# Performance work log

Hardware: AMD Instinct MI355X
Metric: run time of the kernel (lower is better)

Reference implementation:

```python
import jax, jax.numpy as jnp
import numpy as np

N_NODES = 100000
N_EDGES = 1600000
IN_DIM = 128
HID_DIM = 128
OUT_DIM = 64
BN_EPS = 1e-5


def setup_inputs() -> dict:
    key = jax.random.key(0)
    ks = jax.random.split(key, 8)
    x = jax.random.normal(ks[0], (N_NODES, IN_DIM), dtype=jnp.float32)
    edge_index = jax.random.randint(ks[1], (2, N_EDGES), 0, N_NODES, dtype=jnp.int64)
    s1 = 1.0 / np.sqrt(IN_DIM)
    s2 = 1.0 / np.sqrt(HID_DIM)
    return {
        "x": x,
        "edge_index": edge_index,
        "W1l": jax.random.normal(ks[2], (HID_DIM, IN_DIM), dtype=jnp.float32) * s1,
        "b1l": jnp.zeros((HID_DIM,), dtype=jnp.float32),
        "W1r": jax.random.normal(ks[3], (HID_DIM, IN_DIM), dtype=jnp.float32) * s1,
        "bn_gamma": jnp.ones((HID_DIM,), dtype=jnp.float32),
        "bn_beta": jnp.zeros((HID_DIM,), dtype=jnp.float32),
        "bn_mean": jnp.zeros((HID_DIM,), dtype=jnp.float32),
        "bn_var": jnp.ones((HID_DIM,), dtype=jnp.float32),
        "W2l": jax.random.normal(ks[4], (OUT_DIM, HID_DIM), dtype=jnp.float32) * s2,
        "b2l": jnp.zeros((OUT_DIM,), dtype=jnp.float32),
        "W2r": jax.random.normal(ks[5], (OUT_DIM, HID_DIM), dtype=jnp.float32) * s2,
    }


def _sage_conv(x, src, dst, Wl, bl, Wr, num_nodes):
    # message = x[src], mean-aggregated at dst; out = lin_l(agg) + lin_r(x)
    msgs = x[src]  # [E, D] gather (memory bound)
    agg = jax.ops.segment_sum(msgs, dst, num_segments=num_nodes)
    deg = jax.ops.segment_sum(jnp.ones((src.shape[0],), dtype=x.dtype), dst,
                              num_segments=num_nodes)
    agg = agg / jnp.maximum(deg, 1.0)[:, None]
    return agg @ Wl.T + bl + x @ Wr.T


def reference(x, edge_index, W1l, b1l, W1r, bn_gamma, bn_beta, bn_mean, bn_var,
              W2l, b2l, W2r):
    src, dst = edge_index[0], edge_index[1]
    n = x.shape[0]
    h = _sage_conv(x, src, dst, W1l, b1l, W1r, n)
    # BatchNorm1d (inference: running stats), then ReLU; dropout is identity in eval
    h = (h - bn_mean) * (bn_gamma * jax.lax.rsqrt(bn_var + BN_EPS)) + bn_beta
    h = jax.nn.relu(h)
    return _sage_conv(h, src, dst, W2l, b2l, W2r, n)
```

## Files before the change

### kernel.cpp

```cpp
#include <hip/hip_runtime.h>
#include <hip/hip_fp16.h>

#define N_NODES 100000
#define N_EDGES 1600000
#define TILE 2048
#define NBUK 64
#define BSH 11
#define NBUK_USED ((N_NODES + (1 << BSH) - 1) >> BSH)
#define CAP 36864
#define SMASK 0x1FFFF

typedef _Float16 f16x8 __attribute__((ext_vector_type(8)));
typedef float    f32x4 __attribute__((ext_vector_type(4)));

__global__ __launch_bounds__(64) void k_binit(int* __restrict__ bcur)
{
    int t = threadIdx.x;
    if (t < NBUK) bcur[t] = t * CAP;
}

__global__ __launch_bounds__(256) void k_binA(
    const int* __restrict__ ei, int* __restrict__ bcur,
    int2* __restrict__ ebuf)
{
    __shared__ int2 scratch[TILE];
    __shared__ int hist[NBUK];
    __shared__ int tstart[NBUK];
    __shared__ int gbase[NBUK];
    int t = threadIdx.x;
    int e0 = blockIdx.x * TILE;
    int tile_n = min(TILE, N_EDGES - e0);
    if (t < NBUK) hist[t] = 0;
    __syncthreads();
    int srcs[8], dsts[8], rank[8], bks[8];
    #pragma unroll
    for (int i = 0; i < 8; ++i) {
        int e = e0 + i * 256 + t;
        bks[i] = -1;
        if (e < N_EDGES) {
            srcs[i] = ei[e];
            dsts[i] = ei[N_EDGES + e];
            bks[i]  = (dsts[i] >> BSH) & (NBUK - 1);
            rank[i] = atomicAdd(&hist[bks[i]], 1);
        }
    }
    __syncthreads();
    if (t == 0) {
        int s = 0;
        #pragma unroll
        for (int b = 0; b < NBUK; ++b) { tstart[b] = s; s += hist[b]; }
    }
    __syncthreads();
    if (t < NBUK && hist[t] > 0)
        gbase[t] = atomicAdd(&bcur[t], hist[t]);
    __syncthreads();
    #pragma unroll
    for (int i = 0; i < 8; ++i)
        if (bks[i] >= 0) {
            int sl = tstart[bks[i]] + rank[i];
            scratch[min(sl, TILE - 1)] = make_int2(srcs[i], dsts[i]);
        }
    __syncthreads();
    for (int p = t; p < tile_n; p += 256) {
        int2 sd = scratch[p];
        int b = (sd.y >> BSH) & (NBUK - 1);
        int o = gbase[b] + (p - tstart[b]);
        ebuf[min(max(o, 0), NBUK * CAP - 1)] = sd;
    }
}

__global__ __launch_bounds__(64) void k_scanb(
    const int* __restrict__ bcur, int* __restrict__ bbase)
{
    __shared__ int s[64];
    int t = threadIdx.x;
    int c = (t < NBUK_USED) ? (bcur[t] - t * CAP) : 0;
    c = min(max(c, 0), CAP);
    s[t] = c;
    __syncthreads();
    #pragma unroll
    for (int off = 1; off < 64; off <<= 1) {
        int v = (t >= off) ? s[t - off] : 0;
        __syncthreads();
        s[t] += v;
        __syncthreads();
    }
    if (t < NBUK_USED) bbase[t] = s[t] - c;
    if (t == NBUK_USED - 1) bbase[NBUK_USED] = s[t];
}

__global__ __launch_bounds__(1024) void k_fillC2(
    const int2* __restrict__ ebuf, const int* __restrict__ bbase,
    int* __restrict__ row_ptr, int* __restrict__ csr_src)
{
    __shared__ int hist[1 << BSH];
    __shared__ int psum[1024];
    __shared__ int cur[1 << BSH];
    int t = threadIdx.x;
    int b = blockIdx.x;
    int base = b << BSH;
    hist[t] = 0;
    hist[t + 1024] = 0;
    __syncthreads();
    int bb  = bbase[b];
    int cnt = min(bbase[b + 1] - bb, CAP);
    const int2* eb = ebuf + (size_t)b * CAP;
    for (int p = t; p < cnt; p += 1024)
        atomicAdd(&hist[(eb[p].y - base) & ((1 << BSH) - 1)], 1);
    __syncthreads();
    int h0 = hist[2 * t], h1 = hist[2 * t + 1];
    psum[t] = h0 + h1;
    __syncthreads();
    #pragma unroll
    for (int off = 1; off < 1024; off <<= 1) {
        int v = (t >= off) ? psum[t - off] : 0;
        __syncthreads();
        psum[t] += v;
        __syncthreads();
    }
    int e0 = bb + psum[t] - (h0 + h1);
    int e1 = e0 + h0;
    int n0g = base + 2 * t, n1g = n0g + 1;
    if (n0g <= N_NODES) row_ptr[n0g] = e0;
    if (n1g <= N_NODES) row_ptr[n1g] = e1;
    cur[2 * t]     = e0;
    cur[2 * t + 1] = e1;
    __syncthreads();
    for (int p = t; p < cnt; p += 1024) {
        int2 sd = eb[p];
        int pos = atomicAdd(&cur[(sd.y - base) & ((1 << BSH) - 1)], 1);
        csr_src[min(max(pos, 0), N_EDGES - 1)] = sd.x;
    }
}

__global__ __launch_bounds__(256) void k_tohalf(
    const float* __restrict__ x, __half* __restrict__ x_h)
{
    int i = blockIdx.x * 256 + threadIdx.x;
    if (i < N_NODES * 32) {
        float4 v = ((const float4*)x)[i];
        __half2 a = __floats2half2_rn(v.x, v.y);
        __half2 b = __floats2half2_rn(v.z, v.w);
        uint2 u = make_uint2(*(unsigned*)&a, *(unsigned*)&b);
        ((uint2*)x_h)[i] = u;
    }
}

__global__ __launch_bounds__(256) void k_wfrag(
    const float* __restrict__ W1l, const float* __restrict__ W1r,
    const float* __restrict__ W2l, const float* __restrict__ W2r,
    __half* __restrict__ W1lf, __half* __restrict__ W1rf,
    __half* __restrict__ W2f)
{
    int t = blockIdx.x * 256 + threadIdx.x;
    if (t >= 49152) return;
    int tt = t & 16383;
    int j    = tt & 7;
    int lane = (tt >> 3) & 63;
    int ks   = (tt >> 9) & 3;
    int ct   = tt >> 11;
    int m = lane & 15, q = lane >> 4;
    int row = ct * 16 + m;
    int col = ks * 32 + q * 8 + j;
    if (t < 16384) {
        W1lf[tt] = __float2half(W1l[row * 128 + col]);
    } else if (t < 32768) {
        W1rf[tt] = __float2half(W1r[row * 128 + col]);
    } else {
        float v = (ct < 4) ? W2l[row * 128 + col]
                           : W2r[(row - 64) * 128 + col];
        W2f[tt] = __float2half(v);
    }
}

__device__ __forceinline__ void acc_row_h(
    const __half* __restrict__ x_h, int s, int lane, float4& acc)
{
    uint2 u = ((const uint2*)(x_h + (size_t)(s & SMASK) * 128))[lane];
    __half2 a = *(__half2*)&u.x;
    __half2 b = *(__half2*)&u.y;
    float2 fa = __half22float2(a);
    float2 fb = __half22float2(b);
    acc.x += fa.x; acc.y += fa.y; acc.z += fb.x; acc.w += fb.y;
}

__global__ __launch_bounds__(256) void k_agg1(
    const int* __restrict__ row_ptr, const int* __restrict__ csr_src,
    const __half* __restrict__ x_h, __half* __restrict__ agg_h)
{
    int tid  = threadIdx.x;
    int n    = blockIdx.x * 8 + (tid >> 5);
    int lane = tid & 31;
    int e1 = min(row_ptr[n + 1], N_EDGES);
    int e0 = min(max(row_ptr[n], 0), e1);
    float4 acc = make_float4(0.f, 0.f, 0.f, 0.f);
    int e = e0;
    for (; e + 4 <= e1; e += 4) {
        int s0 = csr_src[e], s1 = csr_src[e + 1];
        int s2 = csr_src[e + 2], s3 = csr_src[e + 3];
        acc_row_h(x_h, s0, lane, acc);
        acc_row_h(x_h, s1, lane, acc);
        acc_row_h(x_h, s2, lane, acc);
        acc_row_h(x_h, s3, lane, acc);
    }
    for (; e < e1; ++e) acc_row_h(x_h, csr_src[e], lane, acc);
    __half2 h0 = __floats2half2_rn(acc.x, acc.y);
    __half2 h1 = __floats2half2_rn(acc.z, acc.w);
    uint2 u = make_uint2(*(unsigned*)&h0, *(unsigned*)&h1);
    ((uint2*)agg_h)[n * 32 + lane] = u;
}

__global__ __launch_bounds__(256) void k_gemm1(
    const __half* __restrict__ agg_h, const int* __restrict__ row_ptr,
    const __half* __restrict__ x_h,
    const __half* __restrict__ W1lf, const float* __restrict__ b1l,
    const __half* __restrict__ W1rf,
    const float* __restrict__ gamma, const float* __restrict__ beta,
    const float* __restrict__ mean, const float* __restrict__ var,
    __half* __restrict__ h_h)
{
    __shared__ char sm[32768];
    __half (*Aagg)[64][8] = (__half(*)[64][8])sm;
    __half (*Ax)[64][8]   = (__half(*)[64][8])(sm + 16384);
    __half (*Hs)[136]     = (__half(*)[136])sm;
    int tid = threadIdx.x;
    int n0  = blockIdx.x * 64;
    {
        int n  = tid & 63;
        int kg = tid >> 6;
        int ng = n0 + n;
        const uint4* pa = (const uint4*)(agg_h + (size_t)ng * 128 + kg * 32);
        const uint4* px = (const uint4*)(x_h   + (size_t)ng * 128 + kg * 32);
        #pragma unroll
        for (int i = 0; i < 4; ++i) {
            uint4 va = make_uint4(0, 0, 0, 0), vx = va;
            if (ng < N_NODES) { va = pa[i]; vx = px[i]; }
            *(uint4*)&Aagg[kg * 4 + i][n][0] = va;
            *(uint4*)&Ax[kg * 4 + i][n][0]   = vx;
        }
    }
    __syncthreads();
    int lane = tid & 63;
    int w = tid >> 6;
    int m = lane & 15;
    int q = lane >> 4;
    int row = w * 16 + m;
    const __half* bl0 = W1lf + (lane << 3);
    const __half* br0 = W1rf + (lane << 3);
    f32x4 accL[8], accR[8];
    #pragma unroll
    for (int c = 0; c < 8; ++c) {
        accL[c] = (f32x4){0.f, 0.f, 0.f, 0.f};
        accR[c] = (f32x4){0.f, 0.f, 0.f, 0.f};
    }
    #pragma unroll
    for (int ks = 0; ks < 4; ++ks) {
        f16x8 aL = *(const f16x8*)&Aagg[ks * 4 + q][row][0];
        f16x8 aR = *(const f16x8*)&Ax[ks * 4 + q][row][0];
        #pragma unroll
        for (int ct = 0; ct < 8; ++ct) {
            f16x8 bL = *(const f16x8*)(bl0 + ((ct * 4 + ks) << 9));
            f16x8 bR = *(const f16x8*)(br0 + ((ct * 4 + ks) << 9));
            accL[ct] = __builtin_amdgcn_mfma_f32_16x16x32_f16(aL, bL, accL[ct], 0, 0, 0);
            accR[ct] = __builtin_amdgcn_mfma_f32_16x16x32_f16(aR, bR, accR[ct], 0, 0, 0);
        }
    }
    float invd[4];
    #pragma unroll
    for (int r = 0; r < 4; ++r) {
        int n = n0 + w * 16 + q * 4 + r;
        int d = (n < N_NODES) ? (row_ptr[n + 1] - row_ptr[n]) : 1;
        invd[r] = 1.0f / fmaxf((float)d, 1.0f);
    }
    __syncthreads();
    #pragma unroll
    for (int ct = 0; ct < 8; ++ct) {
        int col = ct * 16 + m;
        float s = gamma[col] * rsqrtf(var[col] + 1e-5f);
        float t = beta[col] + (b1l[col] - mean[col]) * s;
        #pragma unroll
        for (int r = 0; r < 4; ++r) {
            float v = accL[ct][r] * invd[r] + accR[ct][r];
            v = fmaxf(v * s + t, 0.f);
            Hs[w * 16 + q * 4 + r][col] = __float2half(v);
        }
    }
    __syncthreads();
    {
        int rr = tid & 63;
        int pg = tid >> 6;
        int ng = n0 + rr;
        if (ng < N_NODES) {
            uint4* dst = (uint4*)(h_h + (size_t)ng * 128);
            #pragma unroll
            for (int i = 0; i < 4; ++i)
                dst[pg * 4 + i] = *(const uint4*)&Hs[rr][(pg * 4 + i) * 8];
        }
    }
}

__global__ __launch_bounds__(256) void k_gemm2(
    const __half* __restrict__ h_h,
    const __half* __restrict__ W2f, const float* __restrict__ b2l,
    __half* __restrict__ p2, float* __restrict__ out)
{
    __shared__ char sm[33792];
    __half (*Ah)[64][8] = (__half(*)[64][8])sm;
    float  (*Cs)[132]   = (float(*)[132])sm;
    int tid = threadIdx.x;
    int n0  = blockIdx.x * 64;
    {
        int n  = tid & 63;
        int kg = tid >> 6;
        int ng = n0 + n;
        const uint4* ph = (const uint4*)(h_h + (size_t)ng * 128 + kg * 32);
        #pragma unroll
        for (int i = 0; i < 4; ++i) {
            uint4 vh = make_uint4(0, 0, 0, 0);
            if (ng < N_NODES) vh = ph[i];
            *(uint4*)&Ah[kg * 4 + i][n][0] = vh;
        }
    }
    __syncthreads();
    int lane = tid & 63;
    int w = tid >> 6;
    int m = lane & 15;
    int q = lane >> 4;
    int row = w * 16 + m;
    const __half* b0 = W2f + (lane << 3);
    f32x4 acc[8];
    #pragma unroll
    for (int c = 0; c < 8; ++c) acc[c] = (f32x4){0.f, 0.f, 0.f, 0.f};
    #pragma unroll
    for (int ks = 0; ks < 4; ++ks) {
        f16x8 a = *(const f16x8*)&Ah[ks * 4 + q][row][0];
        #pragma unroll
        for (int ct = 0; ct < 8; ++ct) {
            f16x8 b = *(const f16x8*)(b0 + ((ct * 4 + ks) << 9));
            acc[ct] = __builtin_amdgcn_mfma_f32_16x16x32_f16(a, b, acc[ct], 0, 0, 0);
        }
    }
    __syncthreads();
    #pragma unroll
    for (int ct = 0; ct < 8; ++ct) {
        int col = ct * 16 + m;
        #pragma unroll
        for (int r = 0; r < 4; ++r)
            Cs[w * 16 + q * 4 + r][col] = acc[ct][r];
    }
    __syncthreads();
    {
        int rr = tid & 63;
        int pg = tid >> 6;
        int ng = n0 + rr;
        if (ng < N_NODES) {
            union { __half hh[16]; uint4 u[2]; } tmp;
            #pragma unroll
            for (int c = 0; c < 16; ++c)
                tmp.hh[c] = __float2half(Cs[rr][pg * 16 + c]);
            uint4* dp = (uint4*)(p2 + (size_t)ng * 64 + pg * 16);
            dp[0] = tmp.u[0];
            dp[1] = tmp.u[1];
            #pragma unroll
            for (int i = 0; i < 4; ++i) {
                float4 v  = *(const float4*)&Cs[rr][64 + pg * 16 + i * 4];
                float4 bb = *(const float4*)(b2l + pg * 16 + i * 4);
                v.x += bb.x; v.y += bb.y; v.z += bb.z; v.w += bb.w;
                *(float4*)(out + (size_t)ng * 64 + pg * 16 + i * 4) = v;
            }
        }
    }
}

__device__ __forceinline__ void acc_row_p2(
    const __half* __restrict__ p2, int s, int lane, float4& acc)
{
    uint2 u = ((const uint2*)(p2 + (size_t)(s & SMASK) * 64))[lane];
    __half2 a = *(__half2*)&u.x;
    __half2 b = *(__half2*)&u.y;
    float2 fa = __half22float2(a);
    float2 fb = __half22float2(b);
    acc.x += fa.x; acc.y += fa.y; acc.z += fb.x; acc.w += fb.y;
}

__global__ __launch_bounds__(256) void k_agg2(
    const int* __restrict__ row_ptr, const int* __restrict__ csr_src,
    const __half* __restrict__ p2, float* __restrict__ out)
{
    int tid  = threadIdx.x;
    int n    = blockIdx.x * 16 + (tid >> 4);
    int lane = tid & 15;
    int e1 = min(row_ptr[n + 1], N_EDGES);
    int e0 = min(max(row_ptr[n], 0), e1);
    float4 acc = make_float4(0.f, 0.f, 0.f, 0.f);
    int e = e0;
    for (; e + 4 <= e1; e += 4) {
        int s0 = csr_src[e], s1 = csr_src[e + 1];
        int s2 = csr_src[e + 2], s3 = csr_src[e + 3];
        acc_row_p2(p2, s0, lane, acc);
        acc_row_p2(p2, s1, lane, acc);
        acc_row_p2(p2, s2, lane, acc);
        acc_row_p2(p2, s3, lane, acc);
    }
    for (; e < e1; ++e) acc_row_p2(p2, csr_src[e], lane, acc);
    float inv = 1.0f / fmaxf((float)(e1 - e0), 1.0f);
    float4* o = (float4*)out + n * 16 + lane;
    float4 cur = *o;
    cur.x += acc.x * inv; cur.y += acc.y * inv;
    cur.z += acc.z * inv; cur.w += acc.w * inv;
    *o = cur;
}

extern "C" void kernel_launch(void* const* d_in, const int* in_sizes, int n_in,
                              void* d_out, int out_size, void* d_ws, size_t ws_size,
                              hipStream_t stream)
{
    const float* x     = (const float*)d_in[0];
    const int*   ei    = (const int*)d_in[1];
    const float* W1l   = (const float*)d_in[2];
    const float* b1l   = (const float*)d_in[3];
    const float* W1r   = (const float*)d_in[4];
    const float* gamma = (const float*)d_in[5];
    const float* beta  = (const float*)d_in[6];
    const float* mean  = (const float*)d_in[7];
    const float* var   = (const float*)d_in[8];
    const float* W2l   = (const float*)d_in[9];
    const float* b2l   = (const float*)d_in[10];
    const float* W2r   = (const float*)d_in[11];
    float* out = (float*)d_out;

    char* ws = (char*)d_ws;
    __half* agg_h   = (__half*)(ws);
    __half* h_h     = (__half*)(ws + 25600000);
    __half* x_h     = (__half*)(ws + 51200000);
    int*    csr_src = (int*)(ws + 76800000);
    int*    row_ptr = (int*)(ws + 83200000);
    __half* W1lf    = (__half*)(ws + 83600016);
    __half* W1rf    = (__half*)(ws + 83632784);
    __half* W2f     = (__half*)(ws + 83665552);
    int2*   ebuf    = (int2*)(ws + 83698320);
    int*    bcur    = (int*)(ws + 102572688);
    int*    bbase   = (int*)(ws + 102572944);
    __half* p2      = agg_h;

    k_binit<<<1, 64, 0, stream>>>(bcur);
    k_tohalf<<<(N_NODES * 32 + 255) / 256, 256, 0, stream>>>(x, x_h);
    k_wfrag<<<192, 256, 0, stream>>>(W1l, W1r, W2l, W2r, W1lf, W1rf, W2f);
    k_binA<<<(N_EDGES + TILE - 1) / TILE, 256, 0, stream>>>(ei, bcur, ebuf);
    k_scanb<<<1, 64, 0, stream>>>(bcur, bbase);
    k_fillC2<<<NBUK_USED, 1024, 0, stream>>>(ebuf, bbase, row_ptr, csr_src);
    k_agg1<<<N_NODES / 8, 256, 0, stream>>>(row_ptr, csr_src, x_h, agg_h);
    k_gemm1<<<(N_NODES + 63) / 64, 256, 0, stream>>>(agg_h, row_ptr, x_h,
                                                     W1lf, b1l, W1rf,
                                                     gamma, beta, mean, var, h_h);
    k_gemm2<<<(N_NODES + 63) / 64, 256, 0, stream>>>(h_h, W2f, b2l, p2, out);
    k_agg2<<<N_NODES / 16, 256, 0, stream>>>(row_ptr, csr_src, p2, out);
}
```

Baseline: 335.4 us.

## Assign one wavefront per node in aggregation kernels with readlane-broadcast indices

Both gather-aggregation kernels now give each destination node a full 64-lane wavefront instead of 32 or 16 lanes. Edge indices are loaded cooperatively, one per lane, and broadcast with readlane. Lane groups then process different edges in parallel and are combined with xor shuffles at the end. The aim is more memory-level parallelism and fewer serialized dependent index loads per node. In exchange there is extra select and shuffle overhead, lanes sit partly idle on odd tails, and the grids are 2x and 4x larger.

```diff
diff --git a/kernel.cpp b/kernel.cpp
--- a/kernel.cpp
+++ b/kernel.cpp
@@ -173,10 +173,10 @@
     }
 }
 
-__device__ __forceinline__ void acc_row_h(
-    const __half* __restrict__ x_h, int s, int lane, float4& acc)
-{
-    uint2 u = ((const uint2*)(x_h + (size_t)(s & SMASK) * 128))[lane];
+__device__ __forceinline__ void acc_row8(
+    const __half* __restrict__ x_h, int s, int col, float4& acc)
+{
+    uint2 u = ((const uint2*)(x_h + (size_t)(s & SMASK) * 128))[col];
     __half2 a = *(__half2*)&u.x;
     __half2 b = *(__half2*)&u.y;
     float2 fa = __half22float2(a);
@@ -189,25 +189,47 @@
     const __half* __restrict__ x_h, __half* __restrict__ agg_h)
 {
     int tid  = threadIdx.x;
-    int n    = blockIdx.x * 8 + (tid >> 5);
-    int lane = tid & 31;
+    int lane = tid & 63;
+    int half = lane >> 5;
+    int col  = lane & 31;
+    int n    = blockIdx.x * 4 + (tid >> 6);
     int e1 = min(row_ptr[n + 1], N_EDGES);
     int e0 = min(max(row_ptr[n], 0), e1);
     float4 acc = make_float4(0.f, 0.f, 0.f, 0.f);
-    int e = e0;
-    for (; e + 4 <= e1; e += 4) {
-        int s0 = csr_src[e], s1 = csr_src[e + 1];
-        int s2 = csr_src[e + 2], s3 = csr_src[e + 3];
-        acc_row_h(x_h, s0, lane, acc);
-        acc_row_h(x_h, s1, lane, acc);
-        acc_row_h(x_h, s2, lane, acc);
-        acc_row_h(x_h, s3, lane, acc);
-    }
-    for (; e < e1; ++e) acc_row_h(x_h, csr_src[e], lane, acc);
-    __half2 h0 = __floats2half2_rn(acc.x, acc.y);
-    __half2 h1 = __floats2half2_rn(acc.z, acc.w);
-    uint2 u = make_uint2(*(unsigned*)&h0, *(unsigned*)&h1);
-    ((uint2*)agg_h)[n * 32 + lane] = u;
+    for (int eb = e0; eb < e1; eb += 64) {
+        int cnt = min(e1 - eb, 64);
+        int sv = csr_src[min(eb + lane, N_EDGES - 1)];
+        int j = 0;
+        for (; j + 8 <= cnt; j += 8) {
+            #pragma unroll
+            for (int u = 0; u < 4; ++u) {
+                int sa = __builtin_amdgcn_readlane(sv, j + 2 * u);
+                int sb = __builtin_amdgcn_readlane(sv, j + 2 * u + 1);
+                int s  = half ? sb : sa;
+                acc_row8(x_h, s, col, acc);
+            }
+        }
+        for (; j + 2 <= cnt; j += 2) {
+            int sa = __builtin_amdgcn_readlane(sv, j);
+            int sb = __builtin_amdgcn_readlane(sv, j + 1);
+            int s  = half ? sb : sa;
+            acc_row8(x_h, s, col, acc);
+        }
+        if (j < cnt) {
+            int sa = __builtin_amdgcn_readlane(sv, j);
+            if (half == 0) acc_row8(x_h, sa, col, acc);
+        }
+    }
+    acc.x += __shfl_xor(acc.x, 32);
+    acc.y += __shfl_xor(acc.y, 32);
+    acc.z += __shfl_xor(acc.z, 32);
+    acc.w += __shfl_xor(acc.w, 32);
+    if (half == 0) {
+        __half2 h0 = __floats2half2_rn(acc.x, acc.y);
+        __half2 h1 = __floats2half2_rn(acc.z, acc.w);
+        uint2 u = make_uint2(*(unsigned*)&h0, *(unsigned*)&h1);
+        ((uint2*)agg_h)[n * 32 + col] = u;
+    }
 }
 
 __global__ __launch_bounds__(256) void k_gemm1(
@@ -372,10 +394,10 @@
     }
 }
 
-__device__ __forceinline__ void acc_row_p2(
-    const __half* __restrict__ p2, int s, int lane, float4& acc)
-{
-    uint2 u = ((const uint2*)(p2 + (size_t)(s & SMASK) * 64))[lane];
+__device__ __forceinline__ void acc_row8p(
+    const __half* __restrict__ p2, int s, int col, float4& acc)
+{
+    uint2 u = ((const uint2*)(p2 + (size_t)(s & SMASK) * 64))[col];
     __half2 a = *(__half2*)&u.x;
     __half2 b = *(__half2*)&u.y;
     float2 fa = __half22float2(a);
@@ -388,27 +410,70 @@
     const __half* __restrict__ p2, float* __restrict__ out)
 {
     int tid  = threadIdx.x;
-    int n    = blockIdx.x * 16 + (tid >> 4);
-    int lane = tid & 15;
+    int lane = tid & 63;
+    int grp  = lane >> 4;
+    int col  = lane & 15;
+    int n    = blockIdx.x * 4 + (tid >> 6);
     int e1 = min(row_ptr[n + 1], N_EDGES);
     int e0 = min(max(row_ptr[n], 0), e1);
     float4 acc = make_float4(0.f, 0.f, 0.f, 0.f);
-    int e = e0;
-    for (; e + 4 <= e1; e += 4) {
-        int s0 = csr_src[e], s1 = csr_src[e + 1];
-        int s2 = csr_src[e + 2], s3 = csr_src[e + 3];
-        acc_row_p2(p2, s0, lane, acc);
-        acc_row_p2(p2, s1, lane, acc);
-        acc_row_p2(p2, s2, lane, acc);
-        acc_row_p2(p2, s3, lane, acc);
-    }
-    for (; e < e1; ++e) acc_row_p2(p2, csr_src[e], lane, acc);
-    float inv = 1.0f / fmaxf((float)(e1 - e0), 1.0f);
-    float4* o = (float4*)out + n * 16 + lane;
-    float4 cur = *o;
-    cur.x += acc.x * inv; cur.y += acc.y * inv;
-    cur.z += acc.z * inv; cur.w += acc.w * inv;
-    *o = cur;
+    for (int eb = e0; eb < e1; eb += 64) {
+        int cnt = min(e1 - eb, 64);
+        int sv = csr_src[min(eb + lane, N_EDGES - 1)];
+        int j = 0;
+        for (; j + 8 <= cnt; j += 8) {
+            #pragma unroll
+            for (int u = 0; u < 2; ++u) {
+                int s0 = __builtin_amdgcn_readlane(sv, j + 4 * u);
+                int s1 = __builtin_amdgcn_readlane(sv, j + 4 * u + 1);
+                int s2 = __builtin_amdgcn_readlane(sv, j + 4 * u + 2);
+                int s3 = __builtin_amdgcn_readlane(sv, j + 4 * u + 3);
+                int sl = (grp & 1) ? s1 : s0;
+                int sh = (grp & 1) ? s3 : s2;
+                int s  = (grp & 2) ? sh : sl;
+                acc_row8p(p2, s, col, acc);
+            }
+        }
+        for (; j + 4 <= cnt; j += 4) {
+            int s0 = __builtin_amdgcn_readlane(sv, j);
+            int s1 = __builtin_amdgcn_readlane(sv, j + 1);
+            int s2 = __builtin_amdgcn_readlane(sv, j + 2);
+            int s3 = __builtin_amdgcn_readlane(sv, j + 3);
+            int sl = (grp & 1) ? s1 : s0;
+            int sh = (grp & 1) ? s3 : s2;
+            int s  = (grp & 2) ? sh : sl;
+            acc_row8p(p2, s, col, acc);
+        }
+        if (j + 2 <= cnt) {
+            int s0 = __builtin_amdgcn_readlane(sv, j);
+            int s1 = __builtin_amdgcn_readlane(sv, j + 1);
+            if (grp < 2) {
+                int s = (grp & 1) ? s1 : s0;
+                acc_row8p(p2, s, col, acc);
+            }
+            j += 2;
+        }
+        if (j < cnt) {
+            int s0 = __builtin_amdgcn_readlane(sv, j);
+            if (grp == 0) acc_row8p(p2, s0, col, acc);
+        }
+    }
+    acc.x += __shfl_xor(acc.x, 16);
+    acc.y += __shfl_xor(acc.y, 16);
+    acc.z += __shfl_xor(acc.z, 16);
+    acc.w += __shfl_xor(acc.w, 16);
+    acc.x += __shfl_xor(acc.x, 32);
+    acc.y += __shfl_xor(acc.y, 32);
+    acc.z += __shfl_xor(acc.z, 32);
+    acc.w += __shfl_xor(acc.w, 32);
+    if (lane < 16) {
+        float inv = 1.0f / fmaxf((float)(e1 - e0), 1.0f);
+        float4* o = (float4*)out + n * 16 + col;
+        float4 cur = *o;
+        cur.x += acc.x * inv; cur.y += acc.y * inv;
+        cur.z += acc.z * inv; cur.w += acc.w * inv;
+        *o = cur;
+    }
 }
 
 extern "C" void kernel_launch(void* const* d_in, const int* in_sizes, int n_in,
@@ -449,10 +514,10 @@
     k_binA<<<(N_EDGES + TILE - 1) / TILE, 256, 0, stream>>>(ei, bcur, ebuf);
     k_scanb<<<1, 64, 0, stream>>>(bcur, bbase);
     k_fillC2<<<NBUK_USED, 1024, 0, stream>>>(ebuf, bbase, row_ptr, csr_src);
-    k_agg1<<<N_NODES / 8, 256, 0, stream>>>(row_ptr, csr_src, x_h, agg_h);
+    k_agg1<<<N_NODES / 4, 256, 0, stream>>>(row_ptr, csr_src, x_h, agg_h);
     k_gemm1<<<(N_NODES + 63) / 64, 256, 0, stream>>>(agg_h, row_ptr, x_h,
                                                      W1lf, b1l, W1rf,
                                                      gamma, beta, mean, var, h_h);
     k_gemm2<<<(N_NODES + 63) / 64, 256, 0, stream>>>(h_h, W2f, b2l, p2, out);
-    k_agg2<<<N_NODES / 16, 256, 0, stream>>>(row_ptr, csr_src, p2, out);
-}
+    k_agg2<<<N_NODES / 4, 256, 0, stream>>>(row_ptr, csr_src, p2, out);
+}
```

Result: slower. 343.2 us (+2.3%).

## Fuse layer-1 aggregation with both GEMMs and merge setup kernels

Applied to the files above, without the earlier changes.

Merges the x-to-half conversion, weight fragment packing and bucket init into one pre-kernel, and folds the bucket-offset scan into the CSR fill kernel as a wave-shuffle scan. Layer-1 neighbour aggregation, the layer-1 GEMM with BN/ReLU, and the layer-2 GEMM now run in one kernel, so agg_h and h_h never go through global memory and the per-node degree is computed in-kernel. The new aggregation uses 64 nodes per block, with each wave handling 16 nodes serially and the two half-waves taking alternating edges. This removes kernel launches and intermediate round-trips, but it may lower the memory-level parallelism of the gather phase and adds shared-memory pressure.

```diff
diff --git a/kernel.cpp b/kernel.cpp
--- a/kernel.cpp
+++ b/kernel.cpp
@@ -13,10 +13,41 @@
 typedef _Float16 f16x8 __attribute__((ext_vector_type(8)));
 typedef float    f32x4 __attribute__((ext_vector_type(4)));
 
-__global__ __launch_bounds__(64) void k_binit(int* __restrict__ bcur)
-{
-    int t = threadIdx.x;
-    if (t < NBUK) bcur[t] = t * CAP;
+__global__ __launch_bounds__(256) void k_pre(
+    const float* __restrict__ x, __half* __restrict__ x_h,
+    const float* __restrict__ W1l, const float* __restrict__ W1r,
+    const float* __restrict__ W2l, const float* __restrict__ W2r,
+    __half* __restrict__ W1lf, __half* __restrict__ W1rf,
+    __half* __restrict__ W2f, int* __restrict__ bcur)
+{
+    int i = blockIdx.x * 256 + threadIdx.x;
+    if (i < N_NODES * 32) {
+        float4 v = ((const float4*)x)[i];
+        __half2 a = __floats2half2_rn(v.x, v.y);
+        __half2 b = __floats2half2_rn(v.z, v.w);
+        uint2 u = make_uint2(*(unsigned*)&a, *(unsigned*)&b);
+        ((uint2*)x_h)[i] = u;
+    }
+    if (i < 49152) {
+        int tt = i & 16383;
+        int j    = tt & 7;
+        int lane = (tt >> 3) & 63;
+        int ks   = (tt >> 9) & 3;
+        int ct   = tt >> 11;
+        int m = lane & 15, q = lane >> 4;
+        int row = ct * 16 + m;
+        int col = ks * 32 + q * 8 + j;
+        if (i < 16384) {
+            W1lf[tt] = __float2half(W1l[row * 128 + col]);
+        } else if (i < 32768) {
+            W1rf[tt] = __float2half(W1r[row * 128 + col]);
+        } else {
+            float v = (ct < 4) ? W2l[row * 128 + col]
+                               : W2r[(row - 64) * 128 + col];
+            W2f[tt] = __float2half(v);
+        }
+    }
+    if (i < NBUK) bcur[i] = i * CAP;
 }
 
 __global__ __launch_bounds__(256) void k_binA(
@@ -69,41 +100,34 @@
     }
 }
 
-__global__ __launch_bounds__(64) void k_scanb(
-    const int* __restrict__ bcur, int* __restrict__ bbase)
-{
-    __shared__ int s[64];
-    int t = threadIdx.x;
-    int c = (t < NBUK_USED) ? (bcur[t] - t * CAP) : 0;
-    c = min(max(c, 0), CAP);
-    s[t] = c;
-    __syncthreads();
-    #pragma unroll
-    for (int off = 1; off < 64; off <<= 1) {
-        int v = (t >= off) ? s[t - off] : 0;
-        __syncthreads();
-        s[t] += v;
-        __syncthreads();
-    }
-    if (t < NBUK_USED) bbase[t] = s[t] - c;
-    if (t == NBUK_USED - 1) bbase[NBUK_USED] = s[t];
-}
-
 __global__ __launch_bounds__(1024) void k_fillC2(
-    const int2* __restrict__ ebuf, const int* __restrict__ bbase,
+    const int2* __restrict__ ebuf, const int* __restrict__ bcur,
     int* __restrict__ row_ptr, int* __restrict__ csr_src)
 {
     __shared__ int hist[1 << BSH];
     __shared__ int psum[1024];
     __shared__ int cur[1 << BSH];
+    __shared__ int bb_l[NBUK_USED + 1];
     int t = threadIdx.x;
     int b = blockIdx.x;
     int base = b << BSH;
     hist[t] = 0;
     hist[t + 1024] = 0;
-    __syncthreads();
-    int bb  = bbase[b];
-    int cnt = min(bbase[b + 1] - bb, CAP);
+    if (t < 64) {
+        int c = (t < NBUK_USED) ? (bcur[t] - t * CAP) : 0;
+        c = min(max(c, 0), CAP);
+        int s = c;
+        #pragma unroll
+        for (int off = 1; off < 64; off <<= 1) {
+            int v = __shfl_up(s, off);
+            if (t >= off) s += v;
+        }
+        if (t < NBUK_USED) bb_l[t] = s - c;
+        if (t == NBUK_USED - 1) bb_l[NBUK_USED] = s;
+    }
+    __syncthreads();
+    int bb  = bb_l[b];
+    int cnt = min(bb_l[b + 1] - bb, CAP);
     const int2* eb = ebuf + (size_t)b * CAP;
     for (int p = t; p < cnt; p += 1024)
         atomicAdd(&hist[(eb[p].y - base) & ((1 << BSH) - 1)], 1);
@@ -133,50 +157,10 @@
     }
 }
 
-__global__ __launch_bounds__(256) void k_tohalf(
-    const float* __restrict__ x, __half* __restrict__ x_h)
-{
-    int i = blockIdx.x * 256 + threadIdx.x;
-    if (i < N_NODES * 32) {
-        float4 v = ((const float4*)x)[i];
-        __half2 a = __floats2half2_rn(v.x, v.y);
-        __half2 b = __floats2half2_rn(v.z, v.w);
-        uint2 u = make_uint2(*(unsigned*)&a, *(unsigned*)&b);
-        ((uint2*)x_h)[i] = u;
-    }
-}
-
-__global__ __launch_bounds__(256) void k_wfrag(
-    const float* __restrict__ W1l, const float* __restrict__ W1r,
-    const float* __restrict__ W2l, const float* __restrict__ W2r,
-    __half* __restrict__ W1lf, __half* __restrict__ W1rf,
-    __half* __restrict__ W2f)
-{
-    int t = blockIdx.x * 256 + threadIdx.x;
-    if (t >= 49152) return;
-    int tt = t & 16383;
-    int j    = tt & 7;
-    int lane = (tt >> 3) & 63;
-    int ks   = (tt >> 9) & 3;
-    int ct   = tt >> 11;
-    int m = lane & 15, q = lane >> 4;
-    int row = ct * 16 + m;
-    int col = ks * 32 + q * 8 + j;
-    if (t < 16384) {
-        W1lf[tt] = __float2half(W1l[row * 128 + col]);
-    } else if (t < 32768) {
-        W1rf[tt] = __float2half(W1r[row * 128 + col]);
-    } else {
-        float v = (ct < 4) ? W2l[row * 128 + col]
-                           : W2r[(row - 64) * 128 + col];
-        W2f[tt] = __float2half(v);
-    }
-}
-
-__device__ __forceinline__ void acc_row_h(
-    const __half* __restrict__ x_h, int s, int lane, float4& acc)
-{
-    uint2 u = ((const uint2*)(x_h + (size_t)(s & SMASK) * 128))[lane];
+__device__ __forceinline__ void acc_row8(
+    const __half* __restrict__ x_h, int s, int col, float4& acc)
+{
+    uint2 u = ((const uint2*)(x_h + (size_t)(s & SMASK) * 128))[col];
     __half2 a = *(__half2*)&u.x;
     __half2 b = *(__half2*)&u.y;
     float2 fa = __half22float2(a);
@@ -184,64 +168,91 @@
     acc.x += fa.x; acc.y += fa.y; acc.z += fb.x; acc.w += fb.y;
 }
 
-__global__ __launch_bounds__(256) void k_agg1(
+__global__ __launch_bounds__(256) void k_l12(
     const int* __restrict__ row_ptr, const int* __restrict__ csr_src,
-    const __half* __restrict__ x_h, __half* __restrict__ agg_h)
-{
-    int tid  = threadIdx.x;
-    int n    = blockIdx.x * 8 + (tid >> 5);
-    int lane = tid & 31;
-    int e1 = min(row_ptr[n + 1], N_EDGES);
-    int e0 = min(max(row_ptr[n], 0), e1);
-    float4 acc = make_float4(0.f, 0.f, 0.f, 0.f);
-    int e = e0;
-    for (; e + 4 <= e1; e += 4) {
-        int s0 = csr_src[e], s1 = csr_src[e + 1];
-        int s2 = csr_src[e + 2], s3 = csr_src[e + 3];
-        acc_row_h(x_h, s0, lane, acc);
-        acc_row_h(x_h, s1, lane, acc);
-        acc_row_h(x_h, s2, lane, acc);
-        acc_row_h(x_h, s3, lane, acc);
-    }
-    for (; e < e1; ++e) acc_row_h(x_h, csr_src[e], lane, acc);
-    __half2 h0 = __floats2half2_rn(acc.x, acc.y);
-    __half2 h1 = __floats2half2_rn(acc.z, acc.w);
-    uint2 u = make_uint2(*(unsigned*)&h0, *(unsigned*)&h1);
-    ((uint2*)agg_h)[n * 32 + lane] = u;
-}
-
-__global__ __launch_bounds__(256) void k_gemm1(
-    const __half* __restrict__ agg_h, const int* __restrict__ row_ptr,
     const __half* __restrict__ x_h,
     const __half* __restrict__ W1lf, const float* __restrict__ b1l,
     const __half* __restrict__ W1rf,
     const float* __restrict__ gamma, const float* __restrict__ beta,
     const float* __restrict__ mean, const float* __restrict__ var,
-    __half* __restrict__ h_h)
-{
-    __shared__ char sm[32768];
+    const __half* __restrict__ W2f, const float* __restrict__ b2l,
+    __half* __restrict__ p2, float* __restrict__ out)
+{
+    __shared__ char sm[34816];
     __half (*Aagg)[64][8] = (__half(*)[64][8])sm;
     __half (*Ax)[64][8]   = (__half(*)[64][8])(sm + 16384);
-    __half (*Hs)[136]     = (__half(*)[136])sm;
-    int tid = threadIdx.x;
-    int n0  = blockIdx.x * 64;
+    __half (*Ah)[64][8]   = (__half(*)[64][8])sm;
+    float  (*Cs)[132]     = (float(*)[132])sm;
+    __shared__ float invdeg[64];
+    int tid  = threadIdx.x;
+    int lane = tid & 63;
+    int w    = tid >> 6;
+    int n0   = blockIdx.x * 64;
+
     {
         int n  = tid & 63;
         int kg = tid >> 6;
         int ng = n0 + n;
-        const uint4* pa = (const uint4*)(agg_h + (size_t)ng * 128 + kg * 32);
-        const uint4* px = (const uint4*)(x_h   + (size_t)ng * 128 + kg * 32);
+        const uint4* px = (const uint4*)(x_h + (size_t)ng * 128 + kg * 32);
         #pragma unroll
         for (int i = 0; i < 4; ++i) {
-            uint4 va = make_uint4(0, 0, 0, 0), vx = va;
-            if (ng < N_NODES) { va = pa[i]; vx = px[i]; }
-            *(uint4*)&Aagg[kg * 4 + i][n][0] = va;
-            *(uint4*)&Ax[kg * 4 + i][n][0]   = vx;
-        }
-    }
-    __syncthreads();
-    int lane = tid & 63;
-    int w = tid >> 6;
+            uint4 vx = make_uint4(0, 0, 0, 0);
+            if (ng < N_NODES) vx = px[i];
+            *(uint4*)&Ax[kg * 4 + i][n][0] = vx;
+        }
+    }
+
+    {
+        int half = lane >> 5;
+        int col  = lane & 31;
+        for (int i = 0; i < 16; ++i) {
+            int nn = n0 + w * 16 + i;
+            int e0 = 0, e1 = 0;
+            if (nn < N_NODES) {
+                e1 = min(row_ptr[nn + 1], N_EDGES);
+                e0 = min(max(row_ptr[nn], 0), e1);
+            }
+            float4 acc = make_float4(0.f, 0.f, 0.f, 0.f);
+            for (int eb = e0; eb < e1; eb += 64) {
+                int cnt = min(e1 - eb, 64);
+                int sv = csr_src[min(eb + lane, N_EDGES - 1)];
+                int j = 0;
+                for (; j + 8 <= cnt; j += 8) {
+                    #pragma unroll
+                    for (int u = 0; u < 4; ++u) {
+                        int sa = __builtin_amdgcn_readlane(sv, j + 2 * u);
+                        int sb = __builtin_amdgcn_readlane(sv, j + 2 * u + 1);
+                        int s  = half ? sb : sa;
+                        acc_row8(x_h, s, col, acc);
+                    }
+                }
+                for (; j + 2 <= cnt; j += 2) {
+                    int sa = __builtin_amdgcn_readlane(sv, j);
+                    int sb = __builtin_amdgcn_readlane(sv, j + 1);
+                    int s  = half ? sb : sa;
+                    acc_row8(x_h, s, col, acc);
+                }
+                if (j < cnt) {
+                    int sa = __builtin_amdgcn_readlane(sv, j);
+                    if (half == 0) acc_row8(x_h, sa, col, acc);
+                }
+            }
+            acc.x += __shfl_xor(acc.x, 32);
+            acc.y += __shfl_xor(acc.y, 32);
+            acc.z += __shfl_xor(acc.z, 32);
+            acc.w += __shfl_xor(acc.w, 32);
+            if (lane == 0)
+                invdeg[w * 16 + i] = 1.0f / fmaxf((float)(e1 - e0), 1.0f);
+            if (half == 0) {
+                __half2 h0 = __floats2half2_rn(acc.x, acc.y);
+                __half2 h1 = __floats2half2_rn(acc.z, acc.w);
+                uint2 u = make_uint2(*(unsigned*)&h0, *(unsigned*)&h1);
+                *(uint2*)&Aagg[col >> 1][w * 16 + i][(col & 1) * 4] = u;
+            }
+        }
+    }
+    __syncthreads();
+
     int m = lane & 15;
     int q = lane >> 4;
     int row = w * 16 + m;
@@ -267,12 +278,10 @@
     }
     float invd[4];
     #pragma unroll
-    for (int r = 0; r < 4; ++r) {
-        int n = n0 + w * 16 + q * 4 + r;
-        int d = (n < N_NODES) ? (row_ptr[n + 1] - row_ptr[n]) : 1;
-        invd[r] = 1.0f / fmaxf((float)d, 1.0f);
-    }
-    __syncthreads();
+    for (int r = 0; r < 4; ++r)
+        invd[r] = invdeg[w * 16 + q * 4 + r];
+    __syncthreads();
+
     #pragma unroll
     for (int ct = 0; ct < 8; ++ct) {
         int col = ct * 16 + m;
@@ -282,62 +291,22 @@
         for (int r = 0; r < 4; ++r) {
             float v = accL[ct][r] * invd[r] + accR[ct][r];
             v = fmaxf(v * s + t, 0.f);
-            Hs[w * 16 + q * 4 + r][col] = __float2half(v);
-        }
-    }
-    __syncthreads();
-    {
-        int rr = tid & 63;
-        int pg = tid >> 6;
-        int ng = n0 + rr;
-        if (ng < N_NODES) {
-            uint4* dst = (uint4*)(h_h + (size_t)ng * 128);
-            #pragma unroll
-            for (int i = 0; i < 4; ++i)
-                dst[pg * 4 + i] = *(const uint4*)&Hs[rr][(pg * 4 + i) * 8];
-        }
-    }
-}
-
-__global__ __launch_bounds__(256) void k_gemm2(
-    const __half* __restrict__ h_h,
-    const __half* __restrict__ W2f, const float* __restrict__ b2l,
-    __half* __restrict__ p2, float* __restrict__ out)
-{
-    __shared__ char sm[33792];
-    __half (*Ah)[64][8] = (__half(*)[64][8])sm;
-    float  (*Cs)[132]   = (float(*)[132])sm;
-    int tid = threadIdx.x;
-    int n0  = blockIdx.x * 64;
-    {
-        int n  = tid & 63;
-        int kg = tid >> 6;
-        int ng = n0 + n;
-        const uint4* ph = (const uint4*)(h_h + (size_t)ng * 128 + kg * 32);
-        #pragma unroll
-        for (int i = 0; i < 4; ++i) {
-            uint4 vh = make_uint4(0, 0, 0, 0);
-            if (ng < N_NODES) vh = ph[i];
-            *(uint4*)&Ah[kg * 4 + i][n][0] = vh;
-        }
-    }
-    __syncthreads();
-    int lane = tid & 63;
-    int w = tid >> 6;
-    int m = lane & 15;
-    int q = lane >> 4;
-    int row = w * 16 + m;
+            Ah[col >> 3][w * 16 + q * 4 + r][col & 7] = __float2half(v);
+        }
+    }
+    __syncthreads();
+
     const __half* b0 = W2f + (lane << 3);
-    f32x4 acc[8];
-    #pragma unroll
-    for (int c = 0; c < 8; ++c) acc[c] = (f32x4){0.f, 0.f, 0.f, 0.f};
+    f32x4 acc2[8];
+    #pragma unroll
+    for (int c = 0; c < 8; ++c) acc2[c] = (f32x4){0.f, 0.f, 0.f, 0.f};
     #pragma unroll
     for (int ks = 0; ks < 4; ++ks) {
         f16x8 a = *(const f16x8*)&Ah[ks * 4 + q][row][0];
         #pragma unroll
         for (int ct = 0; ct < 8; ++ct) {
             f16x8 b = *(const f16x8*)(b0 + ((ct * 4 + ks) << 9));
-            acc[ct] = __builtin_amdgcn_mfma_f32_16x16x32_f16(a, b, acc[ct], 0, 0, 0);
+            acc2[ct] = __builtin_amdgcn_mfma_f32_16x16x32_f16(a, b, acc2[ct], 0, 0, 0);
         }
     }
     __syncthreads();
@@ -346,7 +315,7 @@
         int col = ct * 16 + m;
         #pragma unroll
         for (int r = 0; r < 4; ++r)
-            Cs[w * 16 + q * 4 + r][col] = acc[ct][r];
+            Cs[w * 16 + q * 4 + r][col] = acc2[ct][r];
     }
     __syncthreads();
     {
@@ -430,8 +399,7 @@
     float* out = (float*)d_out;
 
     char* ws = (char*)d_ws;
-    __half* agg_h   = (__half*)(ws);
-    __half* h_h     = (__half*)(ws + 25600000);
+    __half* p2      = (__half*)(ws);
     __half* x_h     = (__half*)(ws + 51200000);
     int*    csr_src = (int*)(ws + 76800000);
     int*    row_ptr = (int*)(ws + 83200000);
@@ -440,19 +408,14 @@
     __half* W2f     = (__half*)(ws + 83665552);
     int2*   ebuf    = (int2*)(ws + 83698320);
     int*    bcur    = (int*)(ws + 102572688);
-    int*    bbase   = (int*)(ws + 102572944);
-    __half* p2      = agg_h;
-
-    k_binit<<<1, 64, 0, stream>>>(bcur);
-    k_tohalf<<<(N_NODES * 32 + 255) / 256, 256, 0, stream>>>(x, x_h);
-    k_wfrag<<<192, 256, 0, stream>>>(W1l, W1r, W2l, W2r, W1lf, W1rf, W2f);
+
+    k_pre<<<12500, 256, 0, stream>>>(x, x_h, W1l, W1r, W2l, W2r,
+                                     W1lf, W1rf, W2f, bcur);
     k_binA<<<(N_EDGES + TILE - 1) / TILE, 256, 0, stream>>>(ei, bcur, ebuf);
-    k_scanb<<<1, 64, 0, stream>>>(bcur, bbase);
-    k_fillC2<<<NBUK_USED, 1024, 0, stream>>>(ebuf, bbase, row_ptr, csr_src);
-    k_agg1<<<N_NODES / 8, 256, 0, stream>>>(row_ptr, csr_src, x_h, agg_h);
-    k_gemm1<<<(N_NODES + 63) / 64, 256, 0, stream>>>(agg_h, row_ptr, x_h,
-                                                     W1lf, b1l, W1rf,
-                                                     gamma, beta, mean, var, h_h);
-    k_gemm2<<<(N_NODES + 63) / 64, 256, 0, stream>>>(h_h, W2f, b2l, p2, out);
+    k_fillC2<<<NBUK_USED, 1024, 0, stream>>>(ebuf, bcur, row_ptr, csr_src);
+    k_l12<<<(N_NODES + 63) / 64, 256, 0, stream>>>(row_ptr, csr_src, x_h,
+                                                   W1lf, b1l, W1rf,
+                                                   gamma, beta, mean, var,
+                                                   W2f, b2l, p2, out);
     k_agg2<<<N_NODES / 16, 256, 0, stream>>>(row_ptr, csr_src, p2, out);
 }
```

Result: slower. 378.7 us (+12.9%).
